# Optimization experiments

Measured on AMD Instinct MI355X. Metric: run time of the kernel, lower is better.

## Reference

```python
import jax, jax.numpy as jnp
import numpy as np

B, T, D_IN = 32, 32, 128
N_SLOTS, M_LEN = 512, 64
NUM_SHIFT, NUM_READ, NUM_WRITE = 3, 4, 1
CTRL_DIM = 256
READ_HEAD_LEN = 3 + M_LEN + NUM_SHIFT            # k, beta, g, s, gamma
WRITE_HEAD_LEN = READ_HEAD_LEN + 2 * M_LEN       # + erase, add vectors
INSTR_DIM = NUM_READ * READ_HEAD_LEN + NUM_WRITE * WRITE_HEAD_LEN


def setup_inputs() -> dict:
    key = jax.random.key(0)
    ks = jax.random.split(key, 4)
    def glorot(k, shape):
        lim = np.sqrt(6.0 / (shape[0] + shape[1])).astype(np.float32)
        return jax.random.uniform(k, shape, jnp.float32, -lim, lim)
    return {
        "x": jax.random.normal(ks[0], (B, T, D_IN), jnp.float32),
        "Wc": glorot(ks[1], (D_IN + NUM_READ * M_LEN, CTRL_DIM)),
        "bc": jnp.zeros((CTRL_DIM,), jnp.float32),
        "heads_kernel": glorot(ks[2], (CTRL_DIM, INSTR_DIM)),
        "heads_bias": jnp.zeros((INSTR_DIM,), jnp.float32),
    }


def _parse_heads(h):
    # h: (B, H, 3 + M + S) -> k, beta, g, s, gamma per _get_weight_vector
    k = h[..., :M_LEN]
    b = jnp.exp(h[..., M_LEN])
    g = jax.nn.sigmoid(h[..., M_LEN + 1])
    s = jax.nn.softmax(h[..., M_LEN + 2:M_LEN + 2 + NUM_SHIFT], axis=-1)
    t = jax.nn.softplus(h[..., M_LEN + 2 + NUM_SHIFT]) + 1.0
    return k, b, g, s, t


def _address(Mem, w_prev, k, b, g, s, t):
    # Mem:(B,N,M) k:(B,H,M) w_prev:(B,H,N) b,g,t:(B,H) s:(B,H,S)
    eps = 1e-8
    Mn = jnp.linalg.norm(Mem, axis=-1)                       # (B,N)
    kn = jnp.linalg.norm(k, axis=-1)                         # (B,H)
    sim = jnp.einsum('bhm,bnm->bhn', k, Mem) / (kn[..., None] * Mn[:, None, :] + eps)
    wc = jax.nn.softmax(b[..., None] * sim, axis=-1)         # content
    wg = g[..., None] * wc + (1.0 - g[..., None]) * w_prev   # gate
    half = NUM_SHIFT // 2                                    # circular shift conv
    wsh = sum(s[..., i:i + 1] * jnp.roll(wg, i - half, axis=-1) for i in range(NUM_SHIFT))
    wt = wsh ** t[..., None]                                 # sharpen
    return wt / (jnp.sum(wt, axis=-1, keepdims=True) + eps)


def _ntm_forward(x, Wc, bc, heads_kernel, heads_bias):
    def step(carry, x_t):
        r, rw, ww, Mem = carry
        # dense controller on [x_t, old read vectors]
        ctrl_in = jnp.concatenate([x_t, r.reshape(B, -1)], axis=-1)
        h = jnp.tanh(ctrl_in @ Wc + bc)                      # controller_out == instr
        instr = h @ heads_kernel + heads_bias                # (B, INSTR_DIM)
        rh = instr[:, :NUM_READ * READ_HEAD_LEN].reshape(B, NUM_READ, READ_HEAD_LEN)
        wh = instr[:, NUM_READ * READ_HEAD_LEN:].reshape(B, NUM_WRITE, WRITE_HEAD_LEN)
        rw_n = _address(Mem, rw, *_parse_heads(rh))
        ww_n = _address(Mem, ww, *_parse_heads(wh[..., :READ_HEAD_LEN]))
        e = wh[..., READ_HEAD_LEN:READ_HEAD_LEN + M_LEN]     # raw erase (no sigmoid, as in source)
        a = wh[..., READ_HEAD_LEN + M_LEN:]                  # raw add
        # erase all heads, then add all heads (source loops erase first)
        Mem = Mem * jnp.prod(1.0 - ww_n[..., :, None] * e[..., None, :], axis=1)
        Mem = Mem + jnp.einsum('bwn,bwm->bnm', ww_n, a)
        r_n = jnp.einsum('bnm,brn->brm', Mem, rw_n)          # read
        return (r_n, rw_n, ww_n, Mem), h

    init = (jnp.zeros((B, NUM_READ, M_LEN), jnp.float32),
            jnp.zeros((B, NUM_READ, N_SLOTS), jnp.float32),
            jnp.zeros((B, NUM_WRITE, N_SLOTS), jnp.float32),
            jnp.zeros((B, N_SLOTS, M_LEN), jnp.float32))
    _, outs = jax.lax.scan(step, init, jnp.swapaxes(x, 0, 1))  # time-major
    return outs[-1]  # return_sequences=False -> last controller output (B, CTRL_DIM)


def reference(x, Wc, bc, heads_kernel, heads_bias):
    return _ntm_forward(x, Wc, bc, heads_kernel, heads_bias)
```

## Files before the change

kernel.cpp:

```cpp
#include <hip/hip_runtime.h>
#include <math.h>

#define BB 32
#define TT 32
#define D_INX 128
#define NSLOT 512
#define MLEN 64
#define NREAD 4
#define NHEAD 5
#define CDIM 256
#define IDIM 478
#define RHL 70
#define NT 512

#define HKB_OFF 196608

struct SMem {
    float mem[NSLOT * MLEN];
    float wprev[NHEAD * NSLOT];
    float mn[NSLOT];
    float ctrl[384];
    float h[CDIM];
    float instr[480];
    float k[NHEAD * MLEN];
    float e[MLEN];
    float a[MLEN];
    float u[2560];
};

__device__ __forceinline__ unsigned short f2bf(float f) {
    unsigned u = __float_as_uint(f);
    return (unsigned short)((u + 0x7fffu + ((u >> 16) & 1u)) >> 16);
}

__global__ void pack_kernel(const float* __restrict__ Wc, const float* __restrict__ Hk,
                            unsigned short* __restrict__ wctb, unsigned short* __restrict__ hkb)
{
    int idx = blockIdx.x * 256 + threadIdx.x;
    if (idx < 384 * 256) {
        int i = idx >> 8, col = idx & 255;
        wctb[((i >> 3) * 256 + col) * 8 + (i & 7)] = f2bf(Wc[idx]);
    }
    if (idx < 256 * 478) {
        int i = idx / 478, col = idx - i * 478;
        hkb[((i >> 3) * 478 + col) * 8 + (i & 7)] = f2bf(Hk[idx]);
    }
}

#define BF8_DOT(wv, c0, c1, c2, c3, acc) do {                                   \
    unsigned _u0 = __float_as_uint((wv).x), _u1 = __float_as_uint((wv).y);      \
    unsigned _u2 = __float_as_uint((wv).z), _u3 = __float_as_uint((wv).w);      \
    acc += __uint_as_float(_u0 << 16) * (c0).x + __uint_as_float(_u0 & 0xffff0000u) * (c0).y; \
    acc += __uint_as_float(_u1 << 16) * (c1).x + __uint_as_float(_u1 & 0xffff0000u) * (c1).y; \
    acc += __uint_as_float(_u2 << 16) * (c2).x + __uint_as_float(_u2 & 0xffff0000u) * (c2).y; \
    acc += __uint_as_float(_u3 << 16) * (c3).x + __uint_as_float(_u3 & 0xffff0000u) * (c3).y; \
} while (0)

__global__ __launch_bounds__(NT, 2)
void ntm_kernel(const float* __restrict__ x,
                const float* __restrict__ bc,
                const float* __restrict__ hb,
                const unsigned short* __restrict__ wctb,
                const unsigned short* __restrict__ hkb,
                float* __restrict__ out)
{
    extern __shared__ float smem_f[];
    SMem* sc = (SMem*)smem_f;

    const int b    = blockIdx.x;
    const int tid  = threadIdx.x;
    const int lane = tid & 63;
    const int wave = tid >> 6;

    const float bcv = (tid < CDIM) ? bc[tid] : 0.f;
    const float hbv = (tid < IDIM) ? hb[tid] : 0.f;

    {
        float4 z4 = make_float4(0.f, 0.f, 0.f, 0.f);
        float4* m4 = (float4*)sc->mem;
        for (int i = tid; i < NSLOT * MLEN / 4; i += NT) m4[i] = z4;
        for (int i = tid; i < NHEAD * NSLOT; i += NT) sc->wprev[i] = 0.f;
        sc->mn[tid] = 0.f;
        if (tid < 384) sc->ctrl[tid] = (tid < D_INX) ? x[(size_t)b * TT * D_INX + tid] : 0.f;
    }
    __syncthreads();

    for (int t = 0; t < TT; ++t) {
        {
            int col = tid & 255, kb = tid >> 8;
            const float4* wq = (const float4*)wctb + kb * 24 * 256 + col;
            const float2* c2 = (const float2*)sc->ctrl + kb * 96;
            float acc = 0.f;
#pragma unroll
            for (int cc = 0; cc < 24; ++cc) {
                float4 wv = wq[cc * 256];
                float2 x0 = c2[cc * 4], x1 = c2[cc * 4 + 1], x2 = c2[cc * 4 + 2], x3 = c2[cc * 4 + 3];
                BF8_DOT(wv, x0, x1, x2, x3, acc);
            }
            sc->u[kb * 256 + col] = acc;
        }
        __syncthreads();

        if (tid < CDIM) {
            float hv = tanhf(bcv + sc->u[tid] + sc->u[256 + tid]);
            sc->h[tid] = hv;
            if (t == TT - 1) out[(size_t)b * CDIM + tid] = hv;
        } else if (tid < 384 && t + 1 < TT) {
            sc->ctrl[tid - 256] = x[((size_t)b * TT + t + 1) * D_INX + (tid - 256)];
        }
        if (t == TT - 1) break;
        __syncthreads();

        if (tid < IDIM) {
            const float4* wq = (const float4*)hkb + tid;
            const float2* h2 = (const float2*)sc->h;
            float acc = hbv;
#pragma unroll
            for (int c = 0; c < 32; ++c) {
                float4 wv = wq[c * 478];
                float2 x0 = h2[c * 4], x1 = h2[c * 4 + 1], x2 = h2[c * 4 + 2], x3 = h2[c * 4 + 3];
                BF8_DOT(wv, x0, x1, x2, x3, acc);
            }
            sc->instr[tid] = acc;
            if (tid < 350) {
                int hh = (tid * 937) >> 16;
                int m = tid - hh * RHL;
                if (m < MLEN) sc->k[hh * MLEN + m] = acc;
            } else if (tid < 414) {
                sc->e[tid - 350] = acc;
            } else {
                sc->a[tid - 414] = acc;
            }
        }
        __syncthreads();

        {
            int n = tid, nx = n & 15;
            const float4* m4 = (const float4*)sc->mem + n * 16;
            const float4* k4 = (const float4*)sc->k;
            float d0 = 0.f, d1 = 0.f, d2 = 0.f, d3 = 0.f, d4 = 0.f;
#pragma unroll
            for (int j = 0; j < 16; ++j) {
                float4 mv = m4[j ^ nx];
                float4 k0 = k4[j], k1 = k4[16 + j], k2 = k4[32 + j], k3 = k4[48 + j], kw = k4[64 + j];
                d0 += mv.x * k0.x + mv.y * k0.y + mv.z * k0.z + mv.w * k0.w;
                d1 += mv.x * k1.x + mv.y * k1.y + mv.z * k1.z + mv.w * k1.w;
                d2 += mv.x * k2.x + mv.y * k2.y + mv.z * k2.z + mv.w * k2.w;
                d3 += mv.x * k3.x + mv.y * k3.y + mv.z * k3.z + mv.w * k3.w;
                d4 += mv.x * kw.x + mv.y * kw.y + mv.z * kw.z + mv.w * kw.w;
            }
            sc->u[n] = d0; sc->u[512 + n] = d1; sc->u[1024 + n] = d2;
            sc->u[1536 + n] = d3; sc->u[2048 + n] = d4;
        }
        __syncthreads();

        if (wave < NHEAD) {
            const int h = wave;
            const float* ins = sc->instr + h * RHL;
            float kv = ins[lane];
            float sq = kv * kv;
#pragma unroll
            for (int off = 32; off; off >>= 1) sq += __shfl_xor(sq, off);
            float kn = sqrtf(sq);
            float beta = __expf(ins[64]);
            float g = 1.f / (1.f + __expf(-ins[65]));
            float v0 = ins[66], v1 = ins[67], v2 = ins[68];
            float mx3 = fmaxf(v0, fmaxf(v1, v2));
            float e0 = __expf(v0 - mx3), e1 = __expf(v1 - mx3), e2 = __expf(v2 - mx3);
            float inv3 = 1.f / (e0 + e1 + e2);
            float s0 = e0 * inv3, s1 = e1 * inv3, s2 = e2 * inv3;
            float tv = ins[69];
            float tp = fmaxf(tv, 0.f) + log1pf(__expf(-fabsf(tv))) + 1.f;

            float uu[8];
#pragma unroll
            for (int j = 0; j < 8; ++j) {
                int slot = j * 64 + lane;
                float d = sc->u[h * NSLOT + slot];
                uu[j] = beta * d / (kn * sc->mn[slot] + 1e-8f);
            }
            float m = uu[0];
#pragma unroll
            for (int j = 1; j < 8; ++j) m = fmaxf(m, uu[j]);
#pragma unroll
            for (int off = 32; off; off >>= 1) m = fmaxf(m, __shfl_xor(m, off));
            float ev[8]; float Z = 0.f;
#pragma unroll
            for (int j = 0; j < 8; ++j) { ev[j] = __expf(uu[j] - m); Z += ev[j]; }
#pragma unroll
            for (int off = 32; off; off >>= 1) Z += __shfl_xor(Z, off);
            float invZ = 1.f / Z;
            float wg[8];
#pragma unroll
            for (int j = 0; j < 8; ++j) {
                int slot = j * 64 + lane;
                wg[j] = g * ev[j] * invZ + (1.f - g) * sc->wprev[h * NSLOT + slot];
            }
            int lm = (lane + 63) & 63, lp = (lane + 1) & 63;
            float rm[8], rp[8], b63[8], b0[8];
#pragma unroll
            for (int j = 0; j < 8; ++j) {
                rm[j]  = __shfl(wg[j], lm);
                rp[j]  = __shfl(wg[j], lp);
                b63[j] = __shfl(wg[j], 63);
                b0[j]  = __shfl(wg[j], 0);
            }
            if (lane == 0) {
#pragma unroll
                for (int j = 0; j < 8; ++j) rm[j] = b63[(j + 7) & 7];
            }
            if (lane == 63) {
#pragma unroll
                for (int j = 0; j < 8; ++j) rp[j] = b0[(j + 1) & 7];
            }
            float wt[8]; float S = 0.f;
#pragma unroll
            for (int j = 0; j < 8; ++j) {
                float wsh = s0 * rp[j] + s1 * wg[j] + s2 * rm[j];
                wt[j] = __builtin_amdgcn_exp2f(tp * __builtin_amdgcn_logf(wsh));
                S += wt[j];
            }
#pragma unroll
            for (int off = 32; off; off >>= 1) S += __shfl_xor(S, off);
            float invS = 1.f / (S + 1e-8f);
#pragma unroll
            for (int j = 0; j < 8; ++j)
                sc->wprev[h * NSLOT + j * 64 + lane] = wt[j] * invS;
        }
        __syncthreads();

        {
            int n = tid, nx = n & 15;
            float4* m4 = (float4*)sc->mem + n * 16;
            const float4* e4 = (const float4*)sc->e;
            const float4* a4 = (const float4*)sc->a;
            float wv = sc->wprev[4 * NSLOT + n];
            float nsq = 0.f;
#pragma unroll
            for (int j = 0; j < 16; ++j) {
                float4 mv = m4[j ^ nx];
                float4 ev = e4[j], av = a4[j];
                mv.x = mv.x * (1.f - wv * ev.x) + wv * av.x;
                mv.y = mv.y * (1.f - wv * ev.y) + wv * av.y;
                mv.z = mv.z * (1.f - wv * ev.z) + wv * av.z;
                mv.w = mv.w * (1.f - wv * ev.w) + wv * av.w;
                nsq += mv.x * mv.x + mv.y * mv.y + mv.z * mv.z + mv.w * mv.w;
                m4[j ^ nx] = mv;
            }
            sc->mn[n] = sqrtf(nsq);
        }
        __syncthreads();

        {
            int rg = lane >> 4, j = lane & 15;
            int base = wave * 64;
            float4 ac[4];
#pragma unroll
            for (int hh = 0; hh < 4; ++hh) ac[hh] = make_float4(0.f, 0.f, 0.f, 0.f);
#pragma unroll
            for (int i = 0; i < 16; ++i) {
                int n = base + 4 * i + rg;
                float4 mv = ((const float4*)sc->mem)[n * 16 + (j ^ (n & 15))];
                float w0 = sc->wprev[n], w1 = sc->wprev[512 + n];
                float w2 = sc->wprev[1024 + n], w3 = sc->wprev[1536 + n];
                ac[0].x += w0 * mv.x; ac[0].y += w0 * mv.y; ac[0].z += w0 * mv.z; ac[0].w += w0 * mv.w;
                ac[1].x += w1 * mv.x; ac[1].y += w1 * mv.y; ac[1].z += w1 * mv.z; ac[1].w += w1 * mv.w;
                ac[2].x += w2 * mv.x; ac[2].y += w2 * mv.y; ac[2].z += w2 * mv.z; ac[2].w += w2 * mv.w;
                ac[3].x += w3 * mv.x; ac[3].y += w3 * mv.y; ac[3].z += w3 * mv.z; ac[3].w += w3 * mv.w;
            }
            float* af = (float*)ac;
#pragma unroll
            for (int q = 0; q < 16; ++q) {
                af[q] += __shfl_xor(af[q], 16);
                af[q] += __shfl_xor(af[q], 32);
            }
            if (rg == 0) {
                float4* rp = (float4*)(sc->u + wave * 256);
                rp[0 * 16 + j] = ac[0];
                rp[1 * 16 + j] = ac[1];
                rp[2 * 16 + j] = ac[2];
                rp[3 * 16 + j] = ac[3];
            }
        }
        __syncthreads();

        if (tid < 256) {
            float s = 0.f;
#pragma unroll
            for (int w = 0; w < 8; ++w) s += sc->u[w * 256 + tid];
            sc->ctrl[128 + tid] = s;
        }
        __syncthreads();
    }
}

extern "C" void kernel_launch(void* const* d_in, const int* in_sizes, int n_in,
                              void* d_out, int out_size, void* d_ws, size_t ws_size,
                              hipStream_t stream) {
    const float* x  = (const float*)d_in[0];
    const float* Wc = (const float*)d_in[1];
    const float* bc = (const float*)d_in[2];
    const float* Hk = (const float*)d_in[3];
    const float* hb = (const float*)d_in[4];
    float* out = (float*)d_out;

    unsigned short* wctb = (unsigned short*)d_ws;
    unsigned short* hkb  = (unsigned short*)((char*)d_ws + HKB_OFF);

    static_assert(sizeof(SMem) <= 163840, "LDS overflow");
    (void)hipFuncSetAttribute((const void*)ntm_kernel,
                              hipFuncAttributeMaxDynamicSharedMemorySize,
                              (int)sizeof(SMem));

    hipLaunchKernelGGL(pack_kernel, dim3(478), dim3(256), 0, stream, Wc, Hk, wctb, hkb);
    hipLaunchKernelGGL(ntm_kernel, dim3(BB), dim3(NT), sizeof(SMem), stream,
                       x, bc, hb, wctb, hkb, out);
}
```

Baseline: 904.4 us.

## Fuse memory write with read, merge norm into similarity pass, cut barriers

The memory erase/add update is fused into the read-vector pass, and the slot-norm computation moves into the similarity pass that already streams memory. Per-wave read partials are summed with shared-memory atomics into a double-buffered ctrl region instead of a separate reduction step. The controller matmul now has thread pairs split K and combine via shuffle, with tanh applied inline, and the next x_t is loaded into alternating buffers. Together these drop several __syncthreads and one full pass over memory per step. The cost is LDS atomics and a fast tanh approximation.

Measured after the change: 928.7 us. 2.7% more time.

```diff
diff --git a/kernel.cpp b/kernel.cpp
--- a/kernel.cpp
+++ b/kernel.cpp
@@ -19,13 +19,13 @@
     float mem[NSLOT * MLEN];
     float wprev[NHEAD * NSLOT];
     float mn[NSLOT];
-    float ctrl[384];
+    float ctrl[512];
     float h[CDIM];
     float instr[480];
     float k[NHEAD * MLEN];
     float e[MLEN];
     float a[MLEN];
-    float u[2560];
+    float u[NHEAD * NSLOT];
 };
 
 __device__ __forceinline__ unsigned short f2bf(float f) {
@@ -71,8 +71,10 @@
     const int tid  = threadIdx.x;
     const int lane = tid & 63;
     const int wave = tid >> 6;
-
-    const float bcv = (tid < CDIM) ? bc[tid] : 0.f;
+    const int colp = tid >> 1;
+    const int half = tid & 1;
+
+    const float bcv = bc[colp];
     const float hbv = (tid < IDIM) ? hb[tid] : 0.f;
 
     {
@@ -80,47 +82,55 @@
         float4* m4 = (float4*)sc->mem;
         for (int i = tid; i < NSLOT * MLEN / 4; i += NT) m4[i] = z4;
         for (int i = tid; i < NHEAD * NSLOT; i += NT) sc->wprev[i] = 0.f;
-        sc->mn[tid] = 0.f;
-        if (tid < 384) sc->ctrl[tid] = (tid < D_INX) ? x[(size_t)b * TT * D_INX + tid] : 0.f;
+        if (tid < D_INX) sc->ctrl[tid] = x[(size_t)b * TT * D_INX + tid];
+        else             sc->ctrl[tid] = 0.f;
     }
     __syncthreads();
 
     for (int t = 0; t < TT; ++t) {
         {
-            int col = tid & 255, kb = tid >> 8;
-            const float4* wq = (const float4*)wctb + kb * 24 * 256 + col;
-            const float2* c2 = (const float2*)sc->ctrl + kb * 96;
-            float acc = 0.f;
+            const bool xload = (tid < D_INX) && (t + 1 < TT);
+            float xval = 0.f;
+            if (xload) xval = x[((size_t)b * TT + t + 1) * D_INX + tid];
+
+            const float4* wq = (const float4*)wctb + colp;
+            const float2* c2 = (const float2*)sc->ctrl;
+            const int xoff = (t & 1) ? 64 : 0;
+            float accs[4] = {0.f, 0.f, 0.f, 0.f};
 #pragma unroll
             for (int cc = 0; cc < 24; ++cc) {
-                float4 wv = wq[cc * 256];
-                float2 x0 = c2[cc * 4], x1 = c2[cc * 4 + 1], x2 = c2[cc * 4 + 2], x3 = c2[cc * 4 + 3];
-                BF8_DOT(wv, x0, x1, x2, x3, acc);
-            }
-            sc->u[kb * 256 + col] = acc;
-        }
-        __syncthreads();
-
-        if (tid < CDIM) {
-            float hv = tanhf(bcv + sc->u[tid] + sc->u[256 + tid]);
-            sc->h[tid] = hv;
-            if (t == TT - 1) out[(size_t)b * CDIM + tid] = hv;
-        } else if (tid < 384 && t + 1 < TT) {
-            sc->ctrl[tid - 256] = x[((size_t)b * TT + t + 1) * D_INX + (tid - 256)];
+                const int cg = half * 24 + cc;
+                const int cb = (cg < 16) ? (xoff + cg * 4) : (128 + (cg - 16) * 4);
+                float4 wv = wq[cg * 256];
+                float2 x0 = c2[cb], x1 = c2[cb + 1], x2 = c2[cb + 2], x3 = c2[cb + 3];
+                BF8_DOT(wv, x0, x1, x2, x3, accs[cc & 3]);
+            }
+            float s = (accs[0] + accs[1]) + (accs[2] + accs[3]);
+            s += __shfl_xor(s, 1);
+            if (half == 0) {
+                float z = bcv + s;
+                z = fminf(fmaxf(z, -15.f), 15.f);
+                float ex = __expf(2.f * z);
+                float hv = (ex - 1.f) / (ex + 1.f);
+                sc->h[colp] = hv;
+                if (t == TT - 1) out[(size_t)b * CDIM + colp] = hv;
+            }
+            if (xload) sc->ctrl[((t + 1) & 1) * 128 + tid] = xval;
         }
         if (t == TT - 1) break;
         __syncthreads();
 
         if (tid < IDIM) {
-            const float4* wq = (const float4*)hkb + tid;
+            const float4* wq2 = (const float4*)hkb + tid;
             const float2* h2 = (const float2*)sc->h;
-            float acc = hbv;
+            float accs[4] = {0.f, 0.f, 0.f, 0.f};
 #pragma unroll
             for (int c = 0; c < 32; ++c) {
-                float4 wv = wq[c * 478];
+                float4 wv = wq2[c * 478];
                 float2 x0 = h2[c * 4], x1 = h2[c * 4 + 1], x2 = h2[c * 4 + 2], x3 = h2[c * 4 + 3];
-                BF8_DOT(wv, x0, x1, x2, x3, acc);
-            }
+                BF8_DOT(wv, x0, x1, x2, x3, accs[c & 3]);
+            }
+            float acc = hbv + (accs[0] + accs[1]) + (accs[2] + accs[3]);
             sc->instr[tid] = acc;
             if (tid < 350) {
                 int hh = (tid * 937) >> 16;
@@ -135,10 +145,10 @@
         __syncthreads();
 
         {
-            int n = tid, nx = n & 15;
+            const int n = tid, nx = n & 15;
             const float4* m4 = (const float4*)sc->mem + n * 16;
             const float4* k4 = (const float4*)sc->k;
-            float d0 = 0.f, d1 = 0.f, d2 = 0.f, d3 = 0.f, d4 = 0.f;
+            float d0 = 0.f, d1 = 0.f, d2 = 0.f, d3 = 0.f, d4 = 0.f, nsq = 0.f;
 #pragma unroll
             for (int j = 0; j < 16; ++j) {
                 float4 mv = m4[j ^ nx];
@@ -148,9 +158,11 @@
                 d2 += mv.x * k2.x + mv.y * k2.y + mv.z * k2.z + mv.w * k2.w;
                 d3 += mv.x * k3.x + mv.y * k3.y + mv.z * k3.z + mv.w * k3.w;
                 d4 += mv.x * kw.x + mv.y * kw.y + mv.z * kw.z + mv.w * kw.w;
-            }
-            sc->u[n] = d0; sc->u[512 + n] = d1; sc->u[1024 + n] = d2;
-            sc->u[1536 + n] = d3; sc->u[2048 + n] = d4;
+                nsq += mv.x * mv.x + mv.y * mv.y + mv.z * mv.z + mv.w * mv.w;
+            }
+            sc->u[n] = d0; sc->u[NSLOT + n] = d1; sc->u[2 * NSLOT + n] = d2;
+            sc->u[3 * NSLOT + n] = d3; sc->u[4 * NSLOT + n] = d4;
+            sc->mn[n] = sqrtf(nsq);
         }
         __syncthreads();
 
@@ -197,21 +209,13 @@
                 wg[j] = g * ev[j] * invZ + (1.f - g) * sc->wprev[h * NSLOT + slot];
             }
             int lm = (lane + 63) & 63, lp = (lane + 1) & 63;
-            float rm[8], rp[8], b63[8], b0[8];
+            float rm[8], rp[8];
 #pragma unroll
             for (int j = 0; j < 8; ++j) {
-                rm[j]  = __shfl(wg[j], lm);
-                rp[j]  = __shfl(wg[j], lp);
-                b63[j] = __shfl(wg[j], 63);
-                b0[j]  = __shfl(wg[j], 0);
-            }
-            if (lane == 0) {
-#pragma unroll
-                for (int j = 0; j < 8; ++j) rm[j] = b63[(j + 7) & 7];
-            }
-            if (lane == 63) {
-#pragma unroll
-                for (int j = 0; j < 8; ++j) rp[j] = b0[(j + 1) & 7];
+                float sm = (lane == 63) ? wg[(j + 7) & 7] : wg[j];
+                float sp = (lane == 0)  ? wg[(j + 1) & 7] : wg[j];
+                rm[j] = __shfl(sm, lm);
+                rp[j] = __shfl(sp, lp);
             }
             float wt[8]; float S = 0.f;
 #pragma unroll
@@ -226,43 +230,34 @@
 #pragma unroll
             for (int j = 0; j < 8; ++j)
                 sc->wprev[h * NSLOT + j * 64 + lane] = wt[j] * invS;
+        } else {
+            int idx = (wave - 5) * 64 + lane;
+            sc->ctrl[256 + idx] = 0.f;
+            if (idx < 64) sc->ctrl[448 + idx] = 0.f;
         }
         __syncthreads();
 
         {
-            int n = tid, nx = n & 15;
-            float4* m4 = (float4*)sc->mem + n * 16;
-            const float4* e4 = (const float4*)sc->e;
-            const float4* a4 = (const float4*)sc->a;
-            float wv = sc->wprev[4 * NSLOT + n];
-            float nsq = 0.f;
-#pragma unroll
-            for (int j = 0; j < 16; ++j) {
-                float4 mv = m4[j ^ nx];
-                float4 ev = e4[j], av = a4[j];
+            const int rg = lane >> 4, j = lane & 15, base = wave * 64;
+            const float4 ev = ((const float4*)sc->e)[j];
+            const float4 av = ((const float4*)sc->a)[j];
+            float4* m4 = (float4*)sc->mem;
+            float4 ac[4];
+#pragma unroll
+            for (int hh = 0; hh < 4; ++hh) ac[hh] = make_float4(0.f, 0.f, 0.f, 0.f);
+#pragma unroll
+            for (int i = 0; i < 16; ++i) {
+                const int n = base + 4 * i + rg;
+                const int idx = n * 16 + (j ^ (n & 15));
+                float4 mv = m4[idx];
+                const float wv = sc->wprev[4 * NSLOT + n];
                 mv.x = mv.x * (1.f - wv * ev.x) + wv * av.x;
                 mv.y = mv.y * (1.f - wv * ev.y) + wv * av.y;
                 mv.z = mv.z * (1.f - wv * ev.z) + wv * av.z;
                 mv.w = mv.w * (1.f - wv * ev.w) + wv * av.w;
-                nsq += mv.x * mv.x + mv.y * mv.y + mv.z * mv.z + mv.w * mv.w;
-                m4[j ^ nx] = mv;
-            }
-            sc->mn[n] = sqrtf(nsq);
-        }
-        __syncthreads();
-
-        {
-            int rg = lane >> 4, j = lane & 15;
-            int base = wave * 64;
-            float4 ac[4];
-#pragma unroll
-            for (int hh = 0; hh < 4; ++hh) ac[hh] = make_float4(0.f, 0.f, 0.f, 0.f);
-#pragma unroll
-            for (int i = 0; i < 16; ++i) {
-                int n = base + 4 * i + rg;
-                float4 mv = ((const float4*)sc->mem)[n * 16 + (j ^ (n & 15))];
-                float w0 = sc->wprev[n], w1 = sc->wprev[512 + n];
-                float w2 = sc->wprev[1024 + n], w3 = sc->wprev[1536 + n];
+                m4[idx] = mv;
+                const float w0 = sc->wprev[n],             w1 = sc->wprev[NSLOT + n];
+                const float w2 = sc->wprev[2 * NSLOT + n], w3 = sc->wprev[3 * NSLOT + n];
                 ac[0].x += w0 * mv.x; ac[0].y += w0 * mv.y; ac[0].z += w0 * mv.z; ac[0].w += w0 * mv.w;
                 ac[1].x += w1 * mv.x; ac[1].y += w1 * mv.y; ac[1].z += w1 * mv.z; ac[1].w += w1 * mv.w;
                 ac[2].x += w2 * mv.x; ac[2].y += w2 * mv.y; ac[2].z += w2 * mv.z; ac[2].w += w2 * mv.w;
@@ -275,20 +270,14 @@
                 af[q] += __shfl_xor(af[q], 32);
             }
             if (rg == 0) {
-                float4* rp = (float4*)(sc->u + wave * 256);
-                rp[0 * 16 + j] = ac[0];
-                rp[1 * 16 + j] = ac[1];
-                rp[2 * 16 + j] = ac[2];
-                rp[3 * 16 + j] = ac[3];
-            }
-        }
-        __syncthreads();
-
-        if (tid < 256) {
-            float s = 0.f;
-#pragma unroll
-            for (int w = 0; w < 8; ++w) s += sc->u[w * 256 + tid];
-            sc->ctrl[128 + tid] = s;
+#pragma unroll
+                for (int hh = 0; hh < 4; ++hh) {
+                    atomicAdd(&sc->ctrl[256 + hh * 64 + 4 * j + 0], ac[hh].x);
+                    atomicAdd(&sc->ctrl[256 + hh * 64 + 4 * j + 1], ac[hh].y);
+                    atomicAdd(&sc->ctrl[256 + hh * 64 + 4 * j + 2], ac[hh].z);
+                    atomicAdd(&sc->ctrl[256 + hh * 64 + 4 * j + 3], ac[hh].w);
+                }
+            }
         }
         __syncthreads();
     }
```
